# Kernel tuning notes

Measured on AMD Instinct MI355X. Metric: run time of the kernel, lower is better.

The kernel has to match this reference:

```python
import jax, jax.numpy as jnp
import numpy as np


def setup_inputs() -> dict:
    key = jax.random.key(0)
    ks = jax.random.split(key, 5)
    B, H, W, C = 16, 64, 64, 256
    sd = lambda fan_in: 1.0 / np.sqrt(fan_in)
    return {
        "x": jax.random.normal(ks[0], (B, H, W, C), dtype=jnp.float32),
        "Wf": jax.random.normal(ks[1], (C, C // 8), dtype=jnp.float32) * sd(C),
        "bf": jnp.zeros((C // 8,), dtype=jnp.float32),
        "Wg": jax.random.normal(ks[2], (C, C // 8), dtype=jnp.float32) * sd(C),
        "bg": jnp.zeros((C // 8,), dtype=jnp.float32),
        "Wh": jax.random.normal(ks[3], (C, C // 2), dtype=jnp.float32) * sd(C),
        "bh": jnp.zeros((C // 2,), dtype=jnp.float32),
        "Wo": jax.random.normal(ks[4], (C // 2, C), dtype=jnp.float32) * sd(C // 2),
        "bo": jnp.zeros((C,), dtype=jnp.float32),
    }


def reference(x, Wf, bf, Wg, bg, Wh, bh, Wo, bo):
    B, H, W, C = x.shape
    hw = H * W
    # 1x1 convs == per-pixel channel GEMMs
    f = (jnp.einsum('bhwc,cd->bhwd', x, Wf) + bf).reshape(B, hw, -1)  # keys   [B,hw,C/8]
    g = (jnp.einsum('bhwc,cd->bhwd', x, Wg) + bg).reshape(B, hw, -1)  # queries[B,hw,C/8]
    h = (jnp.einsum('bhwc,cd->bhwd', x, Wh) + bh).reshape(B, hw, -1)  # values [B,hw,C/2]
    # full non-causal spatial attention: s = g @ f^T, softmax over keys, @ h
    s = jnp.einsum('bqd,bkd->bqk', g, f)          # [B,hw,hw]
    beta = jax.nn.softmax(s, axis=-1)
    o = jnp.einsum('bqk,bkd->bqd', beta, h)       # [B,hw,C/2]
    o = o.reshape(B, H, W, C // 2)
    o = jnp.einsum('bhwd,dc->bhwc', o, Wo) + bo   # output 1x1 conv to C
    return x + o
```

## Files before the change

kernel.cpp:

```cpp
#include <hip/hip_runtime.h>
#include <hip/hip_bf16.h>
#include <stdint.h>

typedef __attribute__((ext_vector_type(8))) short short8;
typedef __attribute__((ext_vector_type(4))) float floatx4;
typedef __attribute__((ext_vector_type(16))) float floatx16;
typedef __attribute__((ext_vector_type(4))) int int4v;
typedef __attribute__((ext_vector_type(4))) unsigned int uint4v;
typedef __attribute__((ext_vector_type(2))) unsigned int uint2v;

#define MFMA16(a, b, c) __builtin_amdgcn_mfma_f32_16x16x32_bf16(a, b, c, 0, 0, 0)
#define MFMA32(a, b, c) __builtin_amdgcn_mfma_f32_32x32x16_bf16(a, b, c, 0, 0, 0)

static constexpr int kHW = 4096;
static constexpr int kC  = 256;
static constexpr int kD  = 32;
static constexpr int kDV = 128;

__device__ __forceinline__ short f2bf(float f) {
  union { float f; uint32_t u; } v; v.f = f;
  uint32_t r = (v.u + 0x7FFFu + ((v.u >> 16) & 1u)) >> 16;
  return (short)(uint16_t)r;
}
__device__ __forceinline__ float bf2f(short s) {
  union { uint32_t u; float f; } v; v.u = ((uint32_t)(uint16_t)s) << 16;
  return v.f;
}
__device__ __forceinline__ void split_bf(float f, short& hi, short& lo) {
  hi = f2bf(f);
  lo = f2bf(f - bf2f(hi));
}
__device__ __forceinline__ uint32_t fbits(float f) {
  union { float f; uint32_t u; } v; v.f = f; return v.u;
}
__device__ __forceinline__ uint32_t pk2(float e, float o) {
  return __builtin_amdgcn_perm(fbits(o) + 0x8000u, fbits(e) + 0x8000u, 0x07060302u);
}
__device__ __forceinline__ short8 mkfrag(uint32_t a, uint32_t b, uint32_t c, uint32_t d) {
  uint4v t = {a, b, c, d};
  return __builtin_bit_cast(short8, t);
}

__global__ __launch_bounds__(256) void prep_kernel(
    const float* __restrict__ Wf, const float* __restrict__ Wg,
    const float* __restrict__ Wh, const float* __restrict__ Wo,
    short* __restrict__ Wt_h, short* __restrict__ Wt_l,
    short* __restrict__ Wot_h, short* __restrict__ Wot_l) {
  const int i = blockIdx.x * 256 + threadIdx.x;
  const int total1 = 192 * 256;
  if (i < total1) {
    int c = i >> 8, k = i & 255;
    float wv;
    if (c < 32)       wv = Wf[(size_t)k * 32 + c];
    else if (c < 64)  wv = Wg[(size_t)k * 32 + (c - 32)];
    else              wv = Wh[(size_t)k * 128 + (c - 64)];
    short h, l; split_bf(wv, h, l);
    Wt_h[i] = h; Wt_l[i] = l;
  } else {
    int j = i - total1;
    int c = j >> 7, k = j & 127;
    short h, l; split_bf(Wo[(size_t)k * 256 + c], h, l);
    Wot_h[j] = h; Wot_l[j] = l;
  }
}

__global__ __launch_bounds__(256, 4) void fgh_kernel(
    const float* __restrict__ x,
    const float* __restrict__ bfv, const float* __restrict__ bgv,
    const float* __restrict__ bhv,
    const short* __restrict__ Wt_h, const short* __restrict__ Wt_l,
    short* __restrict__ f_h, short* __restrict__ f_l,
    short* __restrict__ g_h, short* __restrict__ g_l,
    short* __restrict__ hT) {
  __shared__ short ht2[128][72];

  const int tid  = threadIdx.x;
  const int lane = tid & 63;
  const int w    = tid >> 6;
  const int cl   = lane & 15;
  const int row4 = lane >> 4;
  const int px0  = blockIdx.x * 64;

  floatx4 acc[12];
#pragma unroll
  for (int i = 0; i < 12; ++i) acc[i] = (floatx4){0.f, 0.f, 0.f, 0.f};

#pragma unroll
  for (int kp = 0; kp < 8; ++kp) {
    const float* xr = x + (size_t)(px0 + w * 16 + cl) * kC + kp * 32 + row4 * 8;
    float4 v0 = *reinterpret_cast<const float4*>(xr);
    float4 v1 = *reinterpret_cast<const float4*>(xr + 4);
    float vv[8] = {v0.x, v0.y, v0.z, v0.w, v1.x, v1.y, v1.z, v1.w};
    short8 xh, xl;
#pragma unroll
    for (int e = 0; e < 8; ++e) {
      short h, l; split_bf(vv[e], h, l);
      xh[e] = h; xl[e] = l;
    }
#pragma unroll
    for (int ct = 0; ct < 12; ++ct) {
      const size_t woff = (size_t)(ct * 16 + cl) * 256 + kp * 32 + row4 * 8;
      short8 bh_ = *reinterpret_cast<const short8*>(Wt_h + woff);
      short8 bl_ = *reinterpret_cast<const short8*>(Wt_l + woff);
      acc[ct] = MFMA16(xh, bh_, acc[ct]);
      acc[ct] = MFMA16(xh, bl_, acc[ct]);
      acc[ct] = MFMA16(xl, bh_, acc[ct]);
    }
  }

#pragma unroll
  for (int ct = 0; ct < 4; ++ct) {
    int c = ct * 16 + cl;
    float bias = (c < 32) ? bfv[c] : bgv[c - 32];
    const int cc = (c < 32) ? c : (c - 32);
    short* dh = (c < 32) ? f_h : g_h;
    short* dl = (c < 32) ? f_l : g_l;
#pragma unroll
    for (int j = 0; j < 4; ++j) {
      int pix = px0 + w * 16 + row4 * 4 + j;
      short h, l; split_bf(acc[ct][j] + bias, h, l);
      dh[(size_t)pix * kD + cc] = h;
      dl[(size_t)pix * kD + cc] = l;
    }
  }

#pragma unroll
  for (int ct = 4; ct < 12; ++ct) {
    int dv = (ct - 4) * 16 + cl;
    float bias = bhv[dv];
#pragma unroll
    for (int j = 0; j < 4; ++j)
      ht2[dv][w * 16 + row4 * 4 + j] = f2bf(acc[ct][j] + bias);
  }
  __syncthreads();
  const int b   = px0 >> 12;
  const int pb0 = px0 & 4095;
#pragma unroll
  for (int it = 0; it < 4; ++it) {
    int c = tid + it * 256;
    int dv = c >> 3, p8 = c & 7;
    int4v v = *reinterpret_cast<const int4v*>(&ht2[dv][p8 * 8]);
    *reinterpret_cast<int4v*>(hT + ((size_t)(b * kDV + dv)) * kHW + pb0 + p8 * 8) = v;
  }
}

__global__ __launch_bounds__(256, 2) void attn_kernel(
    const short* __restrict__ fkh, const short* __restrict__ fkl,
    const short* __restrict__ gqh, const short* __restrict__ gql,
    const short* __restrict__ hT,
    short* __restrict__ og) {
  __shared__ __align__(16) char smem[65536];

  const int tid  = threadIdx.x;
  const int lane = tid & 63;
  const int w    = tid >> 6;
  const int cl   = lane & 31;
  const int hi   = lane >> 5;
  const int bb   = blockIdx.x >> 5;
  const int q0   = (blockIdx.x & 31) * 128;
  const int qw   = q0 + w * 32;

  const int  sdv  = tid >> 4;
  const int  sk16 = tid & 15;
  const short* hTb = hT + (size_t)bb * kDV * kHW;

  const size_t qbase = ((size_t)bb * kHW + qw + cl) * kD + hi * 8;
  const short8 qh0 = *reinterpret_cast<const short8*>(gqh + qbase);
  const short8 qh1 = *reinterpret_cast<const short8*>(gqh + qbase + 16);
  const short8 ql0 = *reinterpret_cast<const short8*>(gql + qbase);
  const short8 ql1 = *reinterpret_cast<const short8*>(gql + qbase + 16);

  const floatx16 z16 = {0.f,0.f,0.f,0.f,0.f,0.f,0.f,0.f,0.f,0.f,0.f,0.f,0.f,0.f,0.f,0.f};
  floatx16 acc[4];
#pragma unroll
  for (int i = 0; i < 4; ++i) acc[i] = z16;
  float m = -1e30f, ls = 0.f;

  uint4v vr[8];
#pragma unroll
  for (int it = 0; it < 8; ++it) {
    int dv = sdv + it * 16;
    vr[it] = *reinterpret_cast<const uint4v*>(hTb + (size_t)dv * kHW + 0 * 128 + sk16 * 8);
  }
#pragma unroll
  for (int it = 0; it < 8; ++it) {
    int dv = sdv + it * 16;
    *reinterpret_cast<uint4v*>(smem + dv * 256 + ((sk16 * 16) ^ ((dv & 15) << 4))) = vr[it];
  }
#pragma unroll
  for (int it = 0; it < 8; ++it) {
    int dv = sdv + it * 16;
    vr[it] = *reinterpret_cast<const uint4v*>(hTb + (size_t)dv * kHW + 1 * 128 + sk16 * 8);
  }
  __syncthreads();

  for (int kb = 0; kb < 32; ++kb) {
    char* Vb = smem + (kb & 1) * 32768;
    if (kb + 1 < 32) {
      char* Vn = smem + ((kb + 1) & 1) * 32768;
#pragma unroll
      for (int it = 0; it < 8; ++it) {
        int dv = sdv + it * 16;
        *reinterpret_cast<uint4v*>(Vn + dv * 256 + ((sk16 * 16) ^ ((dv & 15) << 4))) = vr[it];
      }
      if (kb + 2 < 32) {
#pragma unroll
        for (int it = 0; it < 8; ++it) {
          int dv = sdv + it * 16;
          vr[it] = *reinterpret_cast<const uint4v*>(
              hTb + (size_t)dv * kHW + (kb + 2) * 128 + sk16 * 8);
        }
      }
    }

#pragma unroll
    for (int t = 0; t < 4; ++t) {
      const int kk = kb * 128 + t * 32;
      const size_t kbse = ((size_t)bb * kHW + kk + cl) * kD + hi * 8;
      short8 kh0 = *reinterpret_cast<const short8*>(fkh + kbse);
      short8 kh1 = *reinterpret_cast<const short8*>(fkh + kbse + 16);
      short8 kl0 = *reinterpret_cast<const short8*>(fkl + kbse);
      short8 kl1 = *reinterpret_cast<const short8*>(fkl + kbse + 16);

      floatx16 s = MFMA32(kh0, qh0, z16);
      s = MFMA32(kh1, qh1, s);
      s = MFMA32(kl0, qh0, s);
      s = MFMA32(kl1, qh1, s);
      s = MFMA32(kh0, ql0, s);
      s = MFMA32(kh1, ql1, s);

      float tm = fmaxf(fmaxf(s[0], s[1]), fmaxf(s[2], s[3]));
      tm = fmaxf(tm, fmaxf(fmaxf(s[4], s[5]), fmaxf(s[6], s[7])));
      float tm2 = fmaxf(fmaxf(s[8], s[9]), fmaxf(s[10], s[11]));
      tm2 = fmaxf(tm2, fmaxf(fmaxf(s[12], s[13]), fmaxf(s[14], s[15])));
      tm = fmaxf(tm, tm2);
      tm = fmaxf(tm, __shfl_xor(tm, 32));

      if (__any(tm > m + 8.0f)) {
        float mn = fmaxf(m, tm);
        float sc = __expf(m - mn);
        ls *= sc;
#pragma unroll
        for (int ct = 0; ct < 4; ++ct)
#pragma unroll
          for (int r = 0; r < 16; ++r) acc[ct][r] *= sc;
        m = mn;
      }

      float pr[16];
      float sum = 0.f;
#pragma unroll
      for (int r = 0; r < 16; ++r) {
        pr[r] = __expf(s[r] - m);
        sum += pr[r];
      }
      ls += sum;

      uint32_t pk[8];
#pragma unroll
      for (int i = 0; i < 8; ++i) pk[i] = pk2(pr[2 * i], pr[2 * i + 1]);
      {
        uint2v r0 = __builtin_amdgcn_permlane32_swap(pk[0], pk[2], false, false);
        pk[0] = r0.x; pk[2] = r0.y;
        uint2v r1 = __builtin_amdgcn_permlane32_swap(pk[1], pk[3], false, false);
        pk[1] = r1.x; pk[3] = r1.y;
        uint2v r2 = __builtin_amdgcn_permlane32_swap(pk[4], pk[6], false, false);
        pk[4] = r2.x; pk[6] = r2.y;
        uint2v r3 = __builtin_amdgcn_permlane32_swap(pk[5], pk[7], false, false);
        pk[5] = r3.x; pk[7] = r3.y;
      }
      short8 pf0 = mkfrag(pk[0], pk[1], pk[2], pk[3]);
      short8 pf1 = mkfrag(pk[4], pk[5], pk[6], pk[7]);

      __builtin_amdgcn_s_setprio(1);
#pragma unroll
      for (int ct = 0; ct < 4; ++ct) {
        int dv = ct * 32 + cl;
        short8 va = *reinterpret_cast<const short8*>(
            Vb + dv * 256 + (((t * 2 + 0) * 32 + hi * 16) ^ ((dv & 15) << 4)));
        acc[ct] = MFMA32(va, pf0, acc[ct]);
      }
#pragma unroll
      for (int ct = 0; ct < 4; ++ct) {
        int dv = ct * 32 + cl;
        short8 va = *reinterpret_cast<const short8*>(
            Vb + dv * 256 + (((t * 2 + 1) * 32 + hi * 16) ^ ((dv & 15) << 4)));
        acc[ct] = MFMA32(va, pf1, acc[ct]);
      }
      __builtin_amdgcn_s_setprio(0);
    }
    __syncthreads();
  }

  ls += __shfl_xor(ls, 32);
  const float inv = 1.0f / ls;

  short* ot = reinterpret_cast<short*>(smem) + w * 32 * 136;
#pragma unroll
  for (int ct = 0; ct < 4; ++ct)
#pragma unroll
    for (int r = 0; r < 16; ++r) {
      int dv = ct * 32 + (r & 3) + 8 * (r >> 2) + 4 * hi;
      ot[cl * 136 + dv] = f2bf(acc[ct][r] * inv);
    }
  __syncthreads();
#pragma unroll
  for (int it = 0; it < 8; ++it) {
    int q2 = it * 4 + (lane >> 4);
    int ck = lane & 15;
    int4v v = *reinterpret_cast<const int4v*>(ot + q2 * 136 + ck * 8);
    *reinterpret_cast<int4v*>(og + ((size_t)bb * kHW + qw + q2) * kDV + ck * 8) = v;
  }
}

__global__ __launch_bounds__(256, 4) void outproj_kernel(
    const short* __restrict__ o,
    const short* __restrict__ Wot_h, const short* __restrict__ Wot_l,
    const float* __restrict__ bo,
    const float* __restrict__ x,
    float* __restrict__ out) {
  const int tid  = threadIdx.x;
  const int lane = tid & 63;
  const int w    = tid >> 6;
  const int cl   = lane & 15;
  const int row4 = lane >> 4;
  const int px0  = blockIdx.x * 64;

  floatx4 acc[16];
#pragma unroll
  for (int i = 0; i < 16; ++i) acc[i] = (floatx4){0.f, 0.f, 0.f, 0.f};

#pragma unroll
  for (int kp = 0; kp < 4; ++kp) {
    short8 a = *reinterpret_cast<const short8*>(
        o + (size_t)(px0 + w * 16 + cl) * kDV + kp * 32 + row4 * 8);
#pragma unroll
    for (int ct = 0; ct < 16; ++ct) {
      const size_t woff = (size_t)(ct * 16 + cl) * 128 + kp * 32 + row4 * 8;
      short8 bh_ = *reinterpret_cast<const short8*>(Wot_h + woff);
      short8 bl_ = *reinterpret_cast<const short8*>(Wot_l + woff);
      acc[ct] = MFMA16(a, bh_, acc[ct]);
      acc[ct] = MFMA16(a, bl_, acc[ct]);
    }
  }

#pragma unroll
  for (int ct = 0; ct < 16; ++ct) {
    int c = ct * 16 + cl;
    float bias = bo[c];
#pragma unroll
    for (int j = 0; j < 4; ++j) {
      size_t idx = (size_t)(px0 + w * 16 + row4 * 4 + j) * kC + c;
      out[idx] = x[idx] + acc[ct][j] + bias;
    }
  }
}

extern "C" void kernel_launch(void* const* d_in, const int* in_sizes, int n_in,
                              void* d_out, int out_size, void* d_ws, size_t ws_size,
                              hipStream_t stream) {
  const float* x  = (const float*)d_in[0];
  const float* Wf = (const float*)d_in[1];
  const float* bf = (const float*)d_in[2];
  const float* Wg = (const float*)d_in[3];
  const float* bg = (const float*)d_in[4];
  const float* Wh = (const float*)d_in[5];
  const float* bh = (const float*)d_in[6];
  const float* Wo = (const float*)d_in[7];
  const float* bo = (const float*)d_in[8];
  float* out = (float*)d_out;

  char* ws = (char*)d_ws;
  const size_t MB = 1024 * 1024;
  short* f_h = (short*)(ws);
  short* f_l = (short*)(ws + 4  * MB);
  short* g_h = (short*)(ws + 8  * MB);
  short* g_l = (short*)(ws + 12 * MB);
  short* hT  = (short*)(ws + 16 * MB);
  short* o   = (short*)(ws + 32 * MB);
  short* Wt_h  = (short*)(ws + 48 * MB);
  short* Wt_l  = (short*)(ws + 48 * MB + 98304);
  short* Wot_h = (short*)(ws + 48 * MB + 196608);
  short* Wot_l = (short*)(ws + 48 * MB + 262144);

  prep_kernel<<<320, 256, 0, stream>>>(Wf, Wg, Wh, Wo, Wt_h, Wt_l, Wot_h, Wot_l);
  fgh_kernel<<<1024, 256, 0, stream>>>(x, bf, bg, bh, Wt_h, Wt_l,
                                       f_h, f_l, g_h, g_l, hT);
  attn_kernel<<<512, 256, 0, stream>>>(f_h, f_l, g_h, g_l, hT, o);
  outproj_kernel<<<1024, 256, 0, stream>>>(o, Wot_h, Wot_l, bo, x, out);
}
```

Before: 450.2 us.

## Split attention over key halves with merge in outproj; retile fgh and use exp2

```diff
diff --git a/kernel.cpp b/kernel.cpp
--- a/kernel.cpp
+++ b/kernel.cpp
@@ -16,6 +16,7 @@
 static constexpr int kC  = 256;
 static constexpr int kD  = 32;
 static constexpr int kDV = 128;
+static constexpr float kLog2e = 1.4426950408889634f;
 
 __device__ __forceinline__ short f2bf(float f) {
   union { float f; uint32_t u; } v; v.f = f;
@@ -64,7 +65,7 @@
   }
 }
 
-__global__ __launch_bounds__(256, 4) void fgh_kernel(
+__global__ __launch_bounds__(256, 3) void fgh_kernel(
     const float* __restrict__ x,
     const float* __restrict__ bfv, const float* __restrict__ bgv,
     const float* __restrict__ bhv,
@@ -72,93 +73,121 @@
     short* __restrict__ f_h, short* __restrict__ f_l,
     short* __restrict__ g_h, short* __restrict__ g_l,
     short* __restrict__ hT) {
-  __shared__ short ht2[128][72];
+  __shared__ short ht2[128][136];
 
   const int tid  = threadIdx.x;
   const int lane = tid & 63;
   const int w    = tid >> 6;
   const int cl   = lane & 15;
   const int row4 = lane >> 4;
-  const int px0  = blockIdx.x * 64;
-
-  floatx4 acc[12];
-#pragma unroll
-  for (int i = 0; i < 12; ++i) acc[i] = (floatx4){0.f, 0.f, 0.f, 0.f};
+  const int px0  = blockIdx.x * 128;
+
+  floatx4 acc[2][12];
+#pragma unroll
+  for (int mt = 0; mt < 2; ++mt)
+#pragma unroll
+    for (int i = 0; i < 12; ++i) acc[mt][i] = (floatx4){0.f, 0.f, 0.f, 0.f};
 
 #pragma unroll
   for (int kp = 0; kp < 8; ++kp) {
-    const float* xr = x + (size_t)(px0 + w * 16 + cl) * kC + kp * 32 + row4 * 8;
-    float4 v0 = *reinterpret_cast<const float4*>(xr);
-    float4 v1 = *reinterpret_cast<const float4*>(xr + 4);
-    float vv[8] = {v0.x, v0.y, v0.z, v0.w, v1.x, v1.y, v1.z, v1.w};
-    short8 xh, xl;
-#pragma unroll
-    for (int e = 0; e < 8; ++e) {
-      short h, l; split_bf(vv[e], h, l);
-      xh[e] = h; xl[e] = l;
-    }
-#pragma unroll
-    for (int ct = 0; ct < 12; ++ct) {
+    short8 xh[2], xl[2];
+#pragma unroll
+    for (int mt = 0; mt < 2; ++mt) {
+      const float* xr = x + (size_t)(px0 + w * 32 + mt * 16 + cl) * kC + kp * 32 + row4 * 8;
+      float4 v0 = *reinterpret_cast<const float4*>(xr);
+      float4 v1 = *reinterpret_cast<const float4*>(xr + 4);
+      float vv[8] = {v0.x, v0.y, v0.z, v0.w, v1.x, v1.y, v1.z, v1.w};
+#pragma unroll
+      for (int e = 0; e < 8; ++e) {
+        short h, l; split_bf(vv[e], h, l);
+        xh[mt][e] = h; xl[mt][e] = l;
+      }
+    }
+#pragma unroll
+    for (int ct = 0; ct < 4; ++ct) {
       const size_t woff = (size_t)(ct * 16 + cl) * 256 + kp * 32 + row4 * 8;
       short8 bh_ = *reinterpret_cast<const short8*>(Wt_h + woff);
       short8 bl_ = *reinterpret_cast<const short8*>(Wt_l + woff);
-      acc[ct] = MFMA16(xh, bh_, acc[ct]);
-      acc[ct] = MFMA16(xh, bl_, acc[ct]);
-      acc[ct] = MFMA16(xl, bh_, acc[ct]);
-    }
-  }
-
-#pragma unroll
-  for (int ct = 0; ct < 4; ++ct) {
-    int c = ct * 16 + cl;
-    float bias = (c < 32) ? bfv[c] : bgv[c - 32];
-    const int cc = (c < 32) ? c : (c - 32);
-    short* dh = (c < 32) ? f_h : g_h;
-    short* dl = (c < 32) ? f_l : g_l;
-#pragma unroll
-    for (int j = 0; j < 4; ++j) {
-      int pix = px0 + w * 16 + row4 * 4 + j;
-      short h, l; split_bf(acc[ct][j] + bias, h, l);
-      dh[(size_t)pix * kD + cc] = h;
-      dl[(size_t)pix * kD + cc] = l;
-    }
-  }
-
-#pragma unroll
-  for (int ct = 4; ct < 12; ++ct) {
-    int dv = (ct - 4) * 16 + cl;
-    float bias = bhv[dv];
-#pragma unroll
-    for (int j = 0; j < 4; ++j)
-      ht2[dv][w * 16 + row4 * 4 + j] = f2bf(acc[ct][j] + bias);
-  }
+#pragma unroll
+      for (int mt = 0; mt < 2; ++mt) {
+        acc[mt][ct] = MFMA16(xh[mt], bh_, acc[mt][ct]);
+        acc[mt][ct] = MFMA16(xh[mt], bl_, acc[mt][ct]);
+        acc[mt][ct] = MFMA16(xl[mt], bh_, acc[mt][ct]);
+      }
+    }
+#pragma unroll
+    for (int ct = 4; ct < 12; ++ct) {
+      const size_t woff = (size_t)(ct * 16 + cl) * 256 + kp * 32 + row4 * 8;
+      short8 bh_ = *reinterpret_cast<const short8*>(Wt_h + woff);
+#pragma unroll
+      for (int mt = 0; mt < 2; ++mt)
+        acc[mt][ct] = MFMA16(xh[mt], bh_, acc[mt][ct]);
+    }
+  }
+
+#pragma unroll
+  for (int mt = 0; mt < 2; ++mt)
+#pragma unroll
+    for (int ct = 0; ct < 4; ++ct) {
+      int c = ct * 16 + cl;
+      const bool isf = (c < 32);
+      float bias = isf ? bfv[c] : bgv[c - 32];
+      const int cc = isf ? c : (c - 32);
+      short* dh = isf ? f_h : g_h;
+      short* dl = isf ? f_l : g_l;
+#pragma unroll
+      for (int j = 0; j < 4; ++j) {
+        int pix = px0 + w * 32 + mt * 16 + row4 * 4 + j;
+        float val = acc[mt][ct][j] + bias;
+        if (isf) val *= kLog2e;
+        short h, l; split_bf(val, h, l);
+        dh[(size_t)pix * kD + cc] = h;
+        dl[(size_t)pix * kD + cc] = l;
+      }
+    }
+
+#pragma unroll
+  for (int mt = 0; mt < 2; ++mt)
+#pragma unroll
+    for (int ct = 4; ct < 12; ++ct) {
+      int dv = (ct - 4) * 16 + cl;
+      float bias = bhv[dv];
+#pragma unroll
+      for (int j = 0; j < 4; ++j)
+        ht2[dv][w * 32 + mt * 16 + row4 * 4 + j] = f2bf(acc[mt][ct][j] + bias);
+    }
   __syncthreads();
   const int b   = px0 >> 12;
   const int pb0 = px0 & 4095;
 #pragma unroll
-  for (int it = 0; it < 4; ++it) {
+  for (int it = 0; it < 8; ++it) {
     int c = tid + it * 256;
-    int dv = c >> 3, p8 = c & 7;
+    int dv = c >> 4, p8 = c & 15;
     int4v v = *reinterpret_cast<const int4v*>(&ht2[dv][p8 * 8]);
     *reinterpret_cast<int4v*>(hT + ((size_t)(b * kDV + dv)) * kHW + pb0 + p8 * 8) = v;
   }
 }
 
-__global__ __launch_bounds__(256, 2) void attn_kernel(
+__global__ __launch_bounds__(256, 4) void attn_kernel(
     const short* __restrict__ fkh, const short* __restrict__ fkl,
     const short* __restrict__ gqh, const short* __restrict__ gql,
     const short* __restrict__ hT,
-    short* __restrict__ og) {
-  __shared__ __align__(16) char smem[65536];
+    short* __restrict__ op,
+    float2* __restrict__ ml) {
+  __shared__ __align__(16) char smem[36864];
 
   const int tid  = threadIdx.x;
   const int lane = tid & 63;
   const int w    = tid >> 6;
   const int cl   = lane & 31;
   const int hi   = lane >> 5;
-  const int bb   = blockIdx.x >> 5;
-  const int q0   = (blockIdx.x & 31) * 128;
+  const int bid  = blockIdx.x;
+  const int bb   = bid >> 6;
+  const int qt   = (bid >> 1) & 31;
+  const int half = bid & 1;
+  const int q0   = qt * 128;
   const int qw   = q0 + w * 32;
+  const int kbase = half * 2048;
 
   const int  sdv  = tid >> 4;
   const int  sk16 = tid & 15;
@@ -180,42 +209,29 @@
 #pragma unroll
   for (int it = 0; it < 8; ++it) {
     int dv = sdv + it * 16;
-    vr[it] = *reinterpret_cast<const uint4v*>(hTb + (size_t)dv * kHW + 0 * 128 + sk16 * 8);
-  }
-#pragma unroll
-  for (int it = 0; it < 8; ++it) {
-    int dv = sdv + it * 16;
-    *reinterpret_cast<uint4v*>(smem + dv * 256 + ((sk16 * 16) ^ ((dv & 15) << 4))) = vr[it];
-  }
-#pragma unroll
-  for (int it = 0; it < 8; ++it) {
-    int dv = sdv + it * 16;
-    vr[it] = *reinterpret_cast<const uint4v*>(hTb + (size_t)dv * kHW + 1 * 128 + sk16 * 8);
-  }
-  __syncthreads();
-
-  for (int kb = 0; kb < 32; ++kb) {
-    char* Vb = smem + (kb & 1) * 32768;
-    if (kb + 1 < 32) {
-      char* Vn = smem + ((kb + 1) & 1) * 32768;
+    vr[it] = *reinterpret_cast<const uint4v*>(hTb + (size_t)dv * kHW + kbase + sk16 * 8);
+  }
+
+  for (int kb = 0; kb < 16; ++kb) {
+    __syncthreads();
+#pragma unroll
+    for (int it = 0; it < 8; ++it) {
+      int dv = sdv + it * 16;
+      *reinterpret_cast<uint4v*>(smem + dv * 256 + ((sk16 * 16) ^ ((dv & 15) << 4))) = vr[it];
+    }
+    if (kb + 1 < 16) {
 #pragma unroll
       for (int it = 0; it < 8; ++it) {
         int dv = sdv + it * 16;
-        *reinterpret_cast<uint4v*>(Vn + dv * 256 + ((sk16 * 16) ^ ((dv & 15) << 4))) = vr[it];
-      }
-      if (kb + 2 < 32) {
-#pragma unroll
-        for (int it = 0; it < 8; ++it) {
-          int dv = sdv + it * 16;
-          vr[it] = *reinterpret_cast<const uint4v*>(
-              hTb + (size_t)dv * kHW + (kb + 2) * 128 + sk16 * 8);
-        }
-      }
-    }
+        vr[it] = *reinterpret_cast<const uint4v*>(
+            hTb + (size_t)dv * kHW + kbase + (kb + 1) * 128 + sk16 * 8);
+      }
+    }
+    __syncthreads();
 
 #pragma unroll
     for (int t = 0; t < 4; ++t) {
-      const int kk = kb * 128 + t * 32;
+      const int kk = kbase + kb * 128 + t * 32;
       const size_t kbse = ((size_t)bb * kHW + kk + cl) * kD + hi * 8;
       short8 kh0 = *reinterpret_cast<const short8*>(fkh + kbse);
       short8 kh1 = *reinterpret_cast<const short8*>(fkh + kbse + 16);
@@ -229,16 +245,17 @@
       s = MFMA32(kh0, ql0, s);
       s = MFMA32(kh1, ql1, s);
 
-      float tm = fmaxf(fmaxf(s[0], s[1]), fmaxf(s[2], s[3]));
-      tm = fmaxf(tm, fmaxf(fmaxf(s[4], s[5]), fmaxf(s[6], s[7])));
-      float tm2 = fmaxf(fmaxf(s[8], s[9]), fmaxf(s[10], s[11]));
-      tm2 = fmaxf(tm2, fmaxf(fmaxf(s[12], s[13]), fmaxf(s[14], s[15])));
-      tm = fmaxf(tm, tm2);
+      float a0 = fmaxf(fmaxf(s[0], s[1]), s[2]);
+      float a1 = fmaxf(fmaxf(s[3], s[4]), s[5]);
+      float a2 = fmaxf(fmaxf(s[6], s[7]), s[8]);
+      float a3 = fmaxf(fmaxf(s[9], s[10]), s[11]);
+      float a4 = fmaxf(fmaxf(s[12], s[13]), s[14]);
+      float tm = fmaxf(fmaxf(fmaxf(a0, a1), a2), fmaxf(fmaxf(a3, a4), s[15]));
       tm = fmaxf(tm, __shfl_xor(tm, 32));
 
-      if (__any(tm > m + 8.0f)) {
+      if (__any(tm > m + 11.5f)) {
         float mn = fmaxf(m, tm);
-        float sc = __expf(m - mn);
+        float sc = __builtin_amdgcn_exp2f(m - mn);
         ls *= sc;
 #pragma unroll
         for (int ct = 0; ct < 4; ++ct)
@@ -251,7 +268,7 @@
       float sum = 0.f;
 #pragma unroll
       for (int r = 0; r < 16; ++r) {
-        pr[r] = __expf(s[r] - m);
+        pr[r] = __builtin_amdgcn_exp2f(s[r] - m);
         sum += pr[r];
       }
       ls += sum;
@@ -277,44 +294,48 @@
       for (int ct = 0; ct < 4; ++ct) {
         int dv = ct * 32 + cl;
         short8 va = *reinterpret_cast<const short8*>(
-            Vb + dv * 256 + (((t * 2 + 0) * 32 + hi * 16) ^ ((dv & 15) << 4)));
+            smem + dv * 256 + (((t * 2 + 0) * 32 + hi * 16) ^ ((dv & 15) << 4)));
         acc[ct] = MFMA32(va, pf0, acc[ct]);
       }
 #pragma unroll
       for (int ct = 0; ct < 4; ++ct) {
         int dv = ct * 32 + cl;
         short8 va = *reinterpret_cast<const short8*>(
-            Vb + dv * 256 + (((t * 2 + 1) * 32 + hi * 16) ^ ((dv & 15) << 4)));
+            smem + dv * 256 + (((t * 2 + 1) * 32 + hi * 16) ^ ((dv & 15) << 4)));
         acc[ct] = MFMA32(va, pf1, acc[ct]);
       }
       __builtin_amdgcn_s_setprio(0);
     }
-    __syncthreads();
   }
 
   ls += __shfl_xor(ls, 32);
   const float inv = 1.0f / ls;
 
-  short* ot = reinterpret_cast<short*>(smem) + w * 32 * 136;
+  __syncthreads();
+  short* ot = reinterpret_cast<short*>(smem) + w * 32 * 132;
 #pragma unroll
   for (int ct = 0; ct < 4; ++ct)
 #pragma unroll
     for (int r = 0; r < 16; ++r) {
       int dv = ct * 32 + (r & 3) + 8 * (r >> 2) + 4 * hi;
-      ot[cl * 136 + dv] = f2bf(acc[ct][r] * inv);
-    }
+      ot[cl * 132 + dv] = f2bf(acc[ct][r] * inv);
+    }
+  if (hi == 0)
+    ml[((size_t)(half * 16 + bb)) * kHW + qw + cl] = make_float2(m, ls);
   __syncthreads();
 #pragma unroll
   for (int it = 0; it < 8; ++it) {
     int q2 = it * 4 + (lane >> 4);
     int ck = lane & 15;
-    int4v v = *reinterpret_cast<const int4v*>(ot + q2 * 136 + ck * 8);
-    *reinterpret_cast<int4v*>(og + ((size_t)bb * kHW + qw + q2) * kDV + ck * 8) = v;
+    int4v v = *reinterpret_cast<const int4v*>(ot + q2 * 132 + ck * 8);
+    *reinterpret_cast<int4v*>(
+        op + (((size_t)(half * 16 + bb)) * kHW + qw + q2) * kDV + ck * 8) = v;
   }
 }
 
 __global__ __launch_bounds__(256, 4) void outproj_kernel(
-    const short* __restrict__ o,
+    const short* __restrict__ op,
+    const float2* __restrict__ ml,
     const short* __restrict__ Wot_h, const short* __restrict__ Wot_l,
     const float* __restrict__ bo,
     const float* __restrict__ x,
@@ -326,14 +347,33 @@
   const int row4 = lane >> 4;
   const int px0  = blockIdx.x * 64;
 
+  const int bbk = px0 >> 12;
+  const int rq  = (px0 & 4095) + w * 16 + cl;
+  float2 e1 = ml[(size_t)bbk * kHW + rq];
+  float2 e2 = ml[((size_t)(16 + bbk)) * kHW + rq];
+  float M  = fmaxf(e1.x, e2.x);
+  float w1 = e1.y * __builtin_amdgcn_exp2f(e1.x - M);
+  float w2 = e2.y * __builtin_amdgcn_exp2f(e2.x - M);
+  float cinv = 1.0f / (w1 + w2);
+  float c1 = w1 * cinv, c2 = w2 * cinv;
+
+  const short* o1 = op + ((size_t)bbk * kHW + rq) * kDV;
+  const short* o2 = op + (((size_t)(16 + bbk)) * kHW + rq) * kDV;
+
   floatx4 acc[16];
 #pragma unroll
   for (int i = 0; i < 16; ++i) acc[i] = (floatx4){0.f, 0.f, 0.f, 0.f};
 
 #pragma unroll
   for (int kp = 0; kp < 4; ++kp) {
-    short8 a = *reinterpret_cast<const short8*>(
-        o + (size_t)(px0 + w * 16 + cl) * kDV + kp * 32 + row4 * 8);
+    short8 a1 = *reinterpret_cast<const short8*>(o1 + kp * 32 + row4 * 8);
+    short8 a2 = *reinterpret_cast<const short8*>(o2 + kp * 32 + row4 * 8);
+    float cv[8];
+#pragma unroll
+    for (int e = 0; e < 8; ++e)
+      cv[e] = c1 * bf2f(a1[e]) + c2 * bf2f(a2[e]);
+    short8 a = mkfrag(pk2(cv[0], cv[1]), pk2(cv[2], cv[3]),
+                      pk2(cv[4], cv[5]), pk2(cv[6], cv[7]));
 #pragma unroll
     for (int ct = 0; ct < 16; ++ct) {
       const size_t woff = (size_t)(ct * 16 + cl) * 128 + kp * 32 + row4 * 8;
@@ -372,20 +412,21 @@
 
   char* ws = (char*)d_ws;
   const size_t MB = 1024 * 1024;
-  short* f_h = (short*)(ws);
-  short* f_l = (short*)(ws + 4  * MB);
-  short* g_h = (short*)(ws + 8  * MB);
-  short* g_l = (short*)(ws + 12 * MB);
-  short* hT  = (short*)(ws + 16 * MB);
-  short* o   = (short*)(ws + 32 * MB);
-  short* Wt_h  = (short*)(ws + 48 * MB);
-  short* Wt_l  = (short*)(ws + 48 * MB + 98304);
-  short* Wot_h = (short*)(ws + 48 * MB + 196608);
-  short* Wot_l = (short*)(ws + 48 * MB + 262144);
+  short*  f_h = (short*)(ws);
+  short*  f_l = (short*)(ws + 4  * MB);
+  short*  g_h = (short*)(ws + 8  * MB);
+  short*  g_l = (short*)(ws + 12 * MB);
+  short*  hT  = (short*)(ws + 16 * MB);
+  short*  op  = (short*)(ws + 32 * MB);
+  float2* ml  = (float2*)(ws + 64 * MB);
+  short* Wt_h  = (short*)(ws + 65 * MB);
+  short* Wt_l  = (short*)(ws + 65 * MB + 98304);
+  short* Wot_h = (short*)(ws + 65 * MB + 196608);
+  short* Wot_l = (short*)(ws + 65 * MB + 262144);
 
   prep_kernel<<<320, 256, 0, stream>>>(Wf, Wg, Wh, Wo, Wt_h, Wt_l, Wot_h, Wot_l);
-  fgh_kernel<<<1024, 256, 0, stream>>>(x, bf, bg, bh, Wt_h, Wt_l,
-                                       f_h, f_l, g_h, g_l, hT);
-  attn_kernel<<<512, 256, 0, stream>>>(f_h, f_l, g_h, g_l, hT, o);
-  outproj_kernel<<<1024, 256, 0, stream>>>(o, Wot_h, Wot_l, bo, x, out);
-}
+  fgh_kernel<<<512, 256, 0, stream>>>(x, bf, bg, bh, Wt_h, Wt_l,
+                                      f_h, f_l, g_h, g_l, hT);
+  attn_kernel<<<1024, 256, 0, stream>>>(f_h, f_l, g_h, g_l, hT, op, ml);
+  outproj_kernel<<<1024, 256, 0, stream>>>(op, ml, Wot_h, Wot_l, bo, x, out);
+}
```

Result: slower. 477.4 us (+6.0%).
